# Kernel tuning notes

Measured on AMD Instinct MI355X. Metric: run time of the kernel, lower is better.

Reference implementation:

```python
import jax, jax.numpy as jnp
import numpy as np

N = 12  # mmse_block_size
REAL_SIZE = N * (N + 1) // 2  # 78: diag + strict lower
IMAG_SIZE = N * (N - 1) // 2  # 66: strict lower only
ROWS, COLS = jnp.tril_indices(N)        # row-major (i, j<=i) matches torch loop order
ROWS_S, COLS_S = jnp.tril_indices(N, -1)  # strict lower, row-major, matches imag loop
DIAG_MASK = jnp.eye(N, dtype=bool)


def _mlp(x, W1, b1, W2, b2, W3, b3):
    h = jax.nn.relu(x @ W1 + b1)
    h = jax.nn.relu(h @ W2 + b2)
    return h @ W3 + b3


def _cholesky_outer(flat):
    # flat: [B, REAL_SIZE + IMAG_SIZE] -> [B, N, N] complex, L @ L^H
    B = flat.shape[0]
    L_real = jnp.zeros((B, N, N), flat.dtype).at[:, ROWS, COLS].set(flat[:, :REAL_SIZE])
    L_real = jnp.where(DIAG_MASK, jax.nn.softplus(L_real), L_real)
    L_imag = jnp.zeros((B, N, N), flat.dtype).at[:, ROWS_S, COLS_S].set(
        flat[:, REAL_SIZE:REAL_SIZE + IMAG_SIZE])
    L = L_real + 1j * L_imag
    return jnp.einsum('bij,bkj->bik', L, jnp.conj(L))


def setup_inputs() -> dict:
    key = jax.random.key(0)
    ks = jax.random.split(key, 13)
    L, H, OUT = 4096, 64, REAL_SIZE + IMAG_SIZE
    sc = lambda k, shp, fan: (jax.random.normal(k, shp, jnp.float32) / np.sqrt(fan))
    return {
        'channel_stats': jax.random.normal(ks[0], (8192, L), jnp.float32),
        'WC1': sc(ks[1], (L, H), L), 'bC1': jnp.zeros((H,), jnp.float32),
        'WC2': sc(ks[2], (H, H), H), 'bC2': jnp.zeros((H,), jnp.float32),
        'WC3': sc(ks[3], (H, OUT), H), 'bC3': jnp.zeros((OUT,), jnp.float32),
        'WR1': sc(ks[4], (L, H), L), 'bR1': jnp.zeros((H,), jnp.float32),
        'WR2': sc(ks[5], (H, H), H), 'bR2': jnp.zeros((H,), jnp.float32),
        'WR3': sc(ks[6], (H, OUT), H), 'bR3': jnp.zeros((OUT,), jnp.float32),
    }


def reference(channel_stats, WC1, bC1, WC2, bC2, WC3, bC3,
              WR1, bR1, WR2, bR2, WR3, bR3):
    C_flat = _mlp(channel_stats, WC1, bC1, WC2, bC2, WC3, bC3)
    R_flat = _mlp(channel_stats, WR1, bR1, WR2, bR2, WR3, bR3)
    C = _cholesky_outer(C_flat)
    R = _cholesky_outer(R_flat)
    return C, R
```

## Files before the change

### kernel.cpp

```cpp
#include <hip/hip_runtime.h>
#include <stdint.h>

#define M_ROWS 8192
#define K_DIM  4096
#define OUTD   144
#define PLANE  1179648
#define NT2    8

typedef __attribute__((ext_vector_type(4))) float  float4v;
typedef __attribute__((ext_vector_type(8))) short  short8v;

static __device__ __forceinline__ unsigned short f2bf(float f) {
    unsigned int u = __builtin_bit_cast(unsigned int, f);
    u += 0x7FFFu + ((u >> 16) & 1u);
    return (unsigned short)(u >> 16);
}

__global__ __launch_bounds__(256) void wt_kernel(
    const float* __restrict__ WC1, const float* __restrict__ WR1,
    unsigned short* __restrict__ Wt) {
    __shared__ float tile[64][65];
    const float* src = (blockIdx.y == 0) ? WC1 : WR1;
    const int k0 = blockIdx.x * 64;
    const int t = threadIdx.x;
    const int j = t & 63, qq = t >> 6;
#pragma unroll
    for (int p = 0; p < 16; ++p) {
        int i = p * 4 + qq;
        tile[i][j] = src[(size_t)(k0 + i) * 64 + j];
    }
    __syncthreads();
    const int tt  = blockIdx.x >> 1;
    const int ksb = (blockIdx.x & 1) * 2;
#pragma unroll
    for (int p = 0; p < 16; ++p) {
        int c = p * 256 + t;
        int e = c & 7, m = (c >> 3) & 15, q = (c >> 7) & 3;
        int ks_l = (c >> 9) & 1, w_l = (c >> 10) & 3;
        int kp = ks_l * 32 + q * 8 + e;
        int np = w_l * 16 + m;
        int wg = blockIdx.y * 4 + w_l;
        size_t dst = ((size_t)(wg * 32 + tt) * 4 + (ksb + ks_l)) * 512
                   + q * 128 + m * 8 + e;
        Wt[dst] = f2bf(tile[kp][np]);
    }
}


#define ISSUE_B(TB_, B0_, B1_, B2_, B3_)                         \
    do { const unsigned short* bp_ = bpw + (size_t)(TB_) * 2048; \
         B0_ = *(const short8v*)(bp_ + 0 * 512);                 \
         B1_ = *(const short8v*)(bp_ + 1 * 512);                 \
         B2_ = *(const short8v*)(bp_ + 2 * 512);                 \
         B3_ = *(const short8v*)(bp_ + 3 * 512); } while (0)

#define ISSUE_A(T_, XA_, XB_, XC_, XD_)                          \
    do { const float* ap_ = xpw + (size_t)(T_) * 512;            \
         XA_ = *(const float4*)(ap_);                            \
         XB_ = *(const float4*)(ap_ + 4);                        \
         XC_ = *(const float4*)(ap_ + 256);                      \
         XD_ = *(const float4*)(ap_ + 260); } while (0)

#define STORE_A(BUF_, XA_, XB_, XC_, XD_)                              \
    do { short8v s1_, s2_;                                             \
         s1_[0] = (short)f2bf((XA_).x); s1_[1] = (short)f2bf((XA_).y); \
         s1_[2] = (short)f2bf((XA_).z); s1_[3] = (short)f2bf((XA_).w); \
         s1_[4] = (short)f2bf((XB_).x); s1_[5] = (short)f2bf((XB_).y); \
         s1_[6] = (short)f2bf((XB_).z); s1_[7] = (short)f2bf((XB_).w); \
         s2_[0] = (short)f2bf((XC_).x); s2_[1] = (short)f2bf((XC_).y); \
         s2_[2] = (short)f2bf((XC_).z); s2_[3] = (short)f2bf((XC_).w); \
         s2_[4] = (short)f2bf((XD_).x); s2_[5] = (short)f2bf((XD_).y); \
         s2_[6] = (short)f2bf((XD_).z); s2_[7] = (short)f2bf((XD_).w); \
         *(short8v*)(Asm_ + (BUF_) * 8192 + (w * 64 + lane) * 8) = s1_; \
         *(short8v*)(Asm_ + (BUF_) * 8192 + 4096 + (w * 64 + lane) * 8) = s2_; } while (0)

#define MFR(BUF_, SUB_, B0_, B1_, B2_, B3_)                                    \
    do { const unsigned short* ab_ = Asm_ + (BUF_) * 8192 + (SUB_) * 2048 + lane * 8; \
         short8v a0_ = *(const short8v*)(ab_ + 0 * 512);                       \
         short8v a1_ = *(const short8v*)(ab_ + 1 * 512);                       \
         short8v a2_ = *(const short8v*)(ab_ + 2 * 512);                       \
         short8v a3_ = *(const short8v*)(ab_ + 3 * 512);                       \
         acc = __builtin_amdgcn_mfma_f32_16x16x32_bf16(a0_, B0_, acc, 0, 0, 0);\
         acc = __builtin_amdgcn_mfma_f32_16x16x32_bf16(a1_, B1_, acc, 0, 0, 0);\
         acc = __builtin_amdgcn_mfma_f32_16x16x32_bf16(a2_, B2_, acc, 0, 0, 0);\
         acc = __builtin_amdgcn_mfma_f32_16x16x32_bf16(a3_, B3_, acc, 0, 0, 0);\
    } while (0)

__global__ __launch_bounds__(512, 8) void gemm1_kernel(
    const float* __restrict__ X, const unsigned short* __restrict__ Wt,
    const float* __restrict__ bC1, const float* __restrict__ bR1,
    unsigned int* __restrict__ O32) {
    __shared__ __align__(16) unsigned short Asm_[2 * 8192];

    const int tid  = threadIdx.x;
    const int lane = tid & 63;
    const int w    = tid >> 6;
    const int r0   = blockIdx.x * 16;
    const int m    = lane & 15, q = lane >> 4;

    float4v acc = {0.f, 0.f, 0.f, 0.f};

    const unsigned short* bpw = Wt + (size_t)w * 32 * 2048 + lane * 8;
    const float* xpw = X + (size_t)(r0 + m) * K_DIM + w * 32 + q * 8;

    short8v b00, b01, b02, b03, b10, b11, b12, b13;
    short8v b20, b21, b22, b23, b30, b31, b32, b33;
    float4 xa0, xa1, xa2, xa3;

    ISSUE_A(0, xa0, xa1, xa2, xa3);

#pragma unroll 1
    for (int t = 0; t < NT2; ++t) {
        const int buf = t & 1;
        STORE_A(buf, xa0, xa1, xa2, xa3);
        if (t + 1 < NT2) ISSUE_A(t + 1, xa0, xa1, xa2, xa3);
        asm volatile("s_waitcnt lgkmcnt(0)" ::: "memory");
        __builtin_amdgcn_s_barrier();
        __builtin_amdgcn_sched_barrier(0);
        ISSUE_B(t * 4 + 0, b00, b01, b02, b03);
        ISSUE_B(t * 4 + 1, b10, b11, b12, b13);
        ISSUE_B(t * 4 + 2, b20, b21, b22, b23);
        ISSUE_B(t * 4 + 3, b30, b31, b32, b33);
        MFR(buf, 0, b00, b01, b02, b03);
        MFR(buf, 1, b10, b11, b12, b13);
        MFR(buf, 2, b20, b21, b22, b23);
        MFR(buf, 3, b30, b31, b32, b33);
    }

    {
        const int c = w * 16 + m;
        const float bv = (c < 64) ? bC1[c] : bR1[c - 64];
#pragma unroll
        for (int i = 0; i < 4; ++i) {
            int r = r0 + q * 4 + i;
            float v = acc[i] + bv; v = v > 0.f ? v : 0.f;
            O32[(size_t)PLANE + (size_t)144 * r + c] =
                __builtin_bit_cast(unsigned int, v);
        }
    }
}

__global__ __launch_bounds__(512, 6) void tail_kernel(
    const float* __restrict__ WC2, const float* __restrict__ bC2,
    const float* __restrict__ WR2, const float* __restrict__ bR2,
    const float* __restrict__ WC3, const float* __restrict__ bC3,
    const float* __restrict__ WR3, const float* __restrict__ bR3,
    unsigned int* __restrict__ O32) {
    __shared__ __align__(16) char smem[41216];
    float* hs  = (float*)smem;
    float* W2s = hs + 16 * 132;
    float* fl  = W2s;

    const int tid = threadIdx.x;
    const int r0  = blockIdx.x * 16;

    {
        int row = tid >> 5, qd = tid & 31;
        const float* h1p =
            (const float*)(O32 + (size_t)PLANE + (size_t)144 * (r0 + row));
        *(float4*)&hs[row * 132 + qd * 4] = *(const float4*)(h1p + qd * 4);
    }
#pragma unroll
    for (int p = 0; p < 4; ++p) {
        int fi = p * 512 + tid;
        int k = fi >> 5, c4 = fi & 31;
        int c = c4 * 4;
        const float* wsrc = (c < 64) ? (WC2 + (size_t)k * 64 + c)
                                     : (WR2 + (size_t)k * 64 + (c - 64));
        *(float4*)&W2s[k * 128 + c] = *(const float4*)wsrc;
    }
    __syncthreads();

    const int rg = tid >> 5;
    const int cg = tid & 31;
    const int koff2 = (cg < 16) ? 0 : 64;
    float acc2[4];
    {
        int c = cg * 4;
        const float* bsrc = (c < 64) ? (bC2 + c) : (bR2 + (c - 64));
#pragma unroll
        for (int j = 0; j < 4; ++j) acc2[j] = bsrc[j];
    }
    for (int k = 0; k < 64; ++k) {
        float4 wv = *(const float4*)&W2s[k * 128 + cg * 4];
        float a = hs[rg * 132 + koff2 + k];
        acc2[0] += a * wv.x; acc2[1] += a * wv.y;
        acc2[2] += a * wv.z; acc2[3] += a * wv.w;
    }
    float4 h2v;
    h2v.x = acc2[0] > 0.f ? acc2[0] : 0.f;
    h2v.y = acc2[1] > 0.f ? acc2[1] : 0.f;
    h2v.z = acc2[2] > 0.f ? acc2[2] : 0.f;
    h2v.w = acc2[3] > 0.f ? acc2[3] : 0.f;
    __syncthreads();
    *(float4*)&hs[rg * 132 + cg * 4] = h2v;
    __syncthreads();

#pragma unroll 1
    for (int pass = 0; pass < 3; ++pass) {
        int c = pass * 128 + cg * 4;
        if (c < 288) {
            const int brn = (c >= 144);
            const int cl = c - (brn ? 144 : 0);
            const float* W3 = brn ? WR3 : WC3;
            const float* b3 = brn ? bR3 : bC3;
            const int ko = brn ? 64 : 0;
            float a3[4];
#pragma unroll
            for (int j = 0; j < 4; ++j) a3[j] = b3[cl + j];
            for (int k = 0; k < 64; ++k) {
                float4 wv = *(const float4*)(W3 + (size_t)k * OUTD + cl);
                float a = hs[rg * 132 + ko + k];
                a3[0] += a * wv.x; a3[1] += a * wv.y;
                a3[2] += a * wv.z; a3[3] += a * wv.w;
            }
            float4 v; v.x = a3[0]; v.y = a3[1]; v.z = a3[2]; v.w = a3[3];
            *(float4*)&fl[rg * 288 + c] = v;
        }
    }
    __syncthreads();

    if (tid < 384) {
        int r = tid / 24, rem = tid % 24;
        int brn = rem / 12, ii = rem % 12;
        float* f = &fl[r * 288 + brn * 144];
        int d = ii * (ii + 1) / 2 + ii;
        float xv = f[d];
        f[d] = (xv > 20.f) ? xv : log1pf(expf(xv));
    }
    __syncthreads();

    for (int task = tid; task < 16 * 2 * 78; task += 512) {
        int r = task / 156, rem = task % 156;
        int brn = rem / 78, p = rem % 78;
        int i = 0;
        while (p >= (i + 1) * (i + 2) / 2) ++i;
        int j = p - i * (i + 1) / 2;
        const float* f = &fl[r * 288 + brn * 144];
        const float* g = f + 78;
        const int ti = i * (i + 1) / 2, tj = j * (j + 1) / 2;
        const int si = i * (i - 1) / 2, sj = j * (j - 1) / 2;
        float re = 0.f, im = 0.f;
        for (int k = 0; k <= j; ++k) {
            float ar_ = f[ti + k];
            float ai  = (k == i) ? 0.f : g[si + k];
            float br_ = f[tj + k];
            float bi  = (k == j) ? 0.f : g[sj + k];
            re += ar_ * br_ + ai * bi;
            im += ai * br_ - ar_ * bi;
        }
        unsigned int reb = (unsigned int)f2bf(re);
        unsigned int imb = (unsigned int)f2bf(im);
        unsigned int imn = (unsigned int)f2bf(-im);
        size_t base = brn ? (size_t)PLANE : 0;
        size_t q1 = (size_t)(r0 + r) * 144 + (size_t)(i * 12 + j);
        O32[base + q1] = imb | (reb << 16);
        if (i != j) {
            size_t q2 = (size_t)(r0 + r) * 144 + (size_t)(j * 12 + i);
            O32[base + q2] = imn | (reb << 16);
        }
    }
}

extern "C" void kernel_launch(void* const* d_in, const int* in_sizes, int n_in,
                              void* d_out, int out_size, void* d_ws, size_t ws_size,
                              hipStream_t stream) {
    const float* X   = (const float*)d_in[0];
    const float* WC1 = (const float*)d_in[1];
    const float* bC1 = (const float*)d_in[2];
    const float* WC2 = (const float*)d_in[3];
    const float* bC2 = (const float*)d_in[4];
    const float* WC3 = (const float*)d_in[5];
    const float* bC3 = (const float*)d_in[6];
    const float* WR1 = (const float*)d_in[7];
    const float* bR1 = (const float*)d_in[8];
    const float* WR2 = (const float*)d_in[9];
    const float* bR2 = (const float*)d_in[10];
    const float* WR3 = (const float*)d_in[11];
    const float* bR3 = (const float*)d_in[12];

    unsigned short* Wt  = (unsigned short*)d_ws;
    unsigned int*   O32 = (unsigned int*)d_out;

    wt_kernel<<<dim3(64, 2), 256, 0, stream>>>(WC1, WR1, Wt);
    gemm1_kernel<<<M_ROWS / 16, 512, 0, stream>>>(X, Wt, bC1, bR1, O32);
    tail_kernel<<<M_ROWS / 16, 512, 0, stream>>>(
        WC2, bC2, WR2, bR2, WC3, bC3, WR3, bR3, O32);
}
```

Measured before the change: 272.6 us.

## Retile first GEMM to 128-row tiles with split-K partials reduced in tail

The first-layer GEMM now gives each block a 128-row by 512-K chunk instead of 16 rows over the full K. Each weight fragment is reused across eight row sub-tiles, which cuts repeated B-matrix global loads. A split-K over eight chunks keeps the grid at 512 blocks. Partial sums go to a workspace buffer and the tail kernel adds them, then applies bias and ReLU. The cost is extra global traffic for the partials (8×8192×128 floats written and read) and fewer waves per SIMD, since launch bounds drop from 8 to 4.

```diff
diff --git a/kernel.cpp b/kernel.cpp
--- a/kernel.cpp
+++ b/kernel.cpp
@@ -5,7 +5,8 @@
 #define K_DIM  4096
 #define OUTD   144
 #define PLANE  1179648
-#define NT2    8
+#define KCH    8
+#define NSTEP  8
 
 typedef __attribute__((ext_vector_type(4))) float  float4v;
 typedef __attribute__((ext_vector_type(8))) short  short8v;
@@ -47,100 +48,105 @@
 }
 
 
-#define ISSUE_B(TB_, B0_, B1_, B2_, B3_)                         \
-    do { const unsigned short* bp_ = bpw + (size_t)(TB_) * 2048; \
-         B0_ = *(const short8v*)(bp_ + 0 * 512);                 \
-         B1_ = *(const short8v*)(bp_ + 1 * 512);                 \
-         B2_ = *(const short8v*)(bp_ + 2 * 512);                 \
-         B3_ = *(const short8v*)(bp_ + 3 * 512); } while (0)
-
-#define ISSUE_A(T_, XA_, XB_, XC_, XD_)                          \
-    do { const float* ap_ = xpw + (size_t)(T_) * 512;            \
-         XA_ = *(const float4*)(ap_);                            \
-         XB_ = *(const float4*)(ap_ + 4);                        \
-         XC_ = *(const float4*)(ap_ + 256);                      \
-         XD_ = *(const float4*)(ap_ + 260); } while (0)
-
-#define STORE_A(BUF_, XA_, XB_, XC_, XD_)                              \
+#define ISSUE_AX(S_, X0_, X1_, X2_, X3_)                       \
+    do { const float* ap_ = xpw + (S_) * 64;                   \
+         X0_ = *(const float4*)(ap_);                          \
+         X1_ = *(const float4*)(ap_ + 4);                      \
+         X2_ = *(const float4*)(ap_ + 32);                     \
+         X3_ = *(const float4*)(ap_ + 36); } while (0)
+
+#define STORE_AX(BUF_, X0_, X1_, X2_, X3_)                             \
     do { short8v s1_, s2_;                                             \
-         s1_[0] = (short)f2bf((XA_).x); s1_[1] = (short)f2bf((XA_).y); \
-         s1_[2] = (short)f2bf((XA_).z); s1_[3] = (short)f2bf((XA_).w); \
-         s1_[4] = (short)f2bf((XB_).x); s1_[5] = (short)f2bf((XB_).y); \
-         s1_[6] = (short)f2bf((XB_).z); s1_[7] = (short)f2bf((XB_).w); \
-         s2_[0] = (short)f2bf((XC_).x); s2_[1] = (short)f2bf((XC_).y); \
-         s2_[2] = (short)f2bf((XC_).z); s2_[3] = (short)f2bf((XC_).w); \
-         s2_[4] = (short)f2bf((XD_).x); s2_[5] = (short)f2bf((XD_).y); \
-         s2_[6] = (short)f2bf((XD_).z); s2_[7] = (short)f2bf((XD_).w); \
-         *(short8v*)(Asm_ + (BUF_) * 8192 + (w * 64 + lane) * 8) = s1_; \
-         *(short8v*)(Asm_ + (BUF_) * 8192 + 4096 + (w * 64 + lane) * 8) = s2_; } while (0)
-
-#define MFR(BUF_, SUB_, B0_, B1_, B2_, B3_)                                    \
-    do { const unsigned short* ab_ = Asm_ + (BUF_) * 8192 + (SUB_) * 2048 + lane * 8; \
-         short8v a0_ = *(const short8v*)(ab_ + 0 * 512);                       \
-         short8v a1_ = *(const short8v*)(ab_ + 1 * 512);                       \
-         short8v a2_ = *(const short8v*)(ab_ + 2 * 512);                       \
-         short8v a3_ = *(const short8v*)(ab_ + 3 * 512);                       \
-         acc = __builtin_amdgcn_mfma_f32_16x16x32_bf16(a0_, B0_, acc, 0, 0, 0);\
-         acc = __builtin_amdgcn_mfma_f32_16x16x32_bf16(a1_, B1_, acc, 0, 0, 0);\
-         acc = __builtin_amdgcn_mfma_f32_16x16x32_bf16(a2_, B2_, acc, 0, 0, 0);\
-         acc = __builtin_amdgcn_mfma_f32_16x16x32_bf16(a3_, B3_, acc, 0, 0, 0);\
-    } while (0)
-
-__global__ __launch_bounds__(512, 8) void gemm1_kernel(
+         s1_[0] = (short)f2bf((X0_).x); s1_[1] = (short)f2bf((X0_).y); \
+         s1_[2] = (short)f2bf((X0_).z); s1_[3] = (short)f2bf((X0_).w); \
+         s1_[4] = (short)f2bf((X1_).x); s1_[5] = (short)f2bf((X1_).y); \
+         s1_[6] = (short)f2bf((X1_).z); s1_[7] = (short)f2bf((X1_).w); \
+         s2_[0] = (short)f2bf((X2_).x); s2_[1] = (short)f2bf((X2_).y); \
+         s2_[2] = (short)f2bf((X2_).z); s2_[3] = (short)f2bf((X2_).w); \
+         s2_[4] = (short)f2bf((X3_).x); s2_[5] = (short)f2bf((X3_).y); \
+         s2_[6] = (short)f2bf((X3_).z); s2_[7] = (short)f2bf((X3_).w); \
+         *(short8v*)(awp + (BUF_) * 8192) = s1_;                       \
+         *(short8v*)(awp + (BUF_) * 8192 + 512) = s2_; } while (0)
+
+#define ISSUE_B2(S_, B0_, B1_)                                   \
+    do { const unsigned short* bp_ = bpw + (size_t)(2 * (S_)) * 512; \
+         B0_ = *(const short8v*)(bp_);                           \
+         B1_ = *(const short8v*)(bp_ + 512); } while (0)
+
+#define MFR2(BUF_, B0_, B1_)                                                   \
+    do { _Pragma("unroll")                                                     \
+         for (int rb = 0; rb < 8; ++rb) {                                      \
+             const unsigned short* ab_ = Asm_ + (BUF_) * 8192 + rb * 1024 + lane * 8; \
+             short8v a0_ = *(const short8v*)(ab_);                             \
+             short8v a1_ = *(const short8v*)(ab_ + 512);                       \
+             acc[rb] = __builtin_amdgcn_mfma_f32_16x16x32_bf16(a0_, B0_, acc[rb], 0, 0, 0); \
+             acc[rb] = __builtin_amdgcn_mfma_f32_16x16x32_bf16(a1_, B1_, acc[rb], 0, 0, 0); \
+         } } while (0)
+
+__global__ __launch_bounds__(512, 4) void gemm1_kernel(
     const float* __restrict__ X, const unsigned short* __restrict__ Wt,
-    const float* __restrict__ bC1, const float* __restrict__ bR1,
-    unsigned int* __restrict__ O32) {
+    float* __restrict__ PART) {
     __shared__ __align__(16) unsigned short Asm_[2 * 8192];
 
     const int tid  = threadIdx.x;
     const int lane = tid & 63;
     const int w    = tid >> 6;
-    const int r0   = blockIdx.x * 16;
     const int m    = lane & 15, q = lane >> 4;
-
-    float4v acc = {0.f, 0.f, 0.f, 0.f};
-
-    const unsigned short* bpw = Wt + (size_t)w * 32 * 2048 + lane * 8;
-    const float* xpw = X + (size_t)(r0 + m) * K_DIM + w * 32 + q * 8;
-
-    short8v b00, b01, b02, b03, b10, b11, b12, b13;
-    short8v b20, b21, b22, b23, b30, b31, b32, b33;
+    const int mt   = blockIdx.x & 63;
+    const int kc   = blockIdx.x >> 6;
+    const int r0   = mt * 128;
+
+    const int srow = tid & 127, sq8 = tid >> 7;
+    const float* xpw = X + (size_t)(r0 + srow) * K_DIM + kc * 512 + sq8 * 8;
+    unsigned short* awp = Asm_ + (srow >> 4) * 1024 + (16 * sq8 + (srow & 15)) * 8;
+
+    const unsigned short* bpw = Wt + (size_t)(w * 128 + kc * 16) * 512 + lane * 8;
+
+    float4v acc[8];
+#pragma unroll
+    for (int rb = 0; rb < 8; ++rb) acc[rb] = (float4v){0.f, 0.f, 0.f, 0.f};
+
     float4 xa0, xa1, xa2, xa3;
-
-    ISSUE_A(0, xa0, xa1, xa2, xa3);
+    short8v bA0, bA1, bB0, bB1;
+
+    ISSUE_AX(0, xa0, xa1, xa2, xa3);
+    ISSUE_B2(0, bA0, bA1);
 
 #pragma unroll 1
-    for (int t = 0; t < NT2; ++t) {
-        const int buf = t & 1;
-        STORE_A(buf, xa0, xa1, xa2, xa3);
-        if (t + 1 < NT2) ISSUE_A(t + 1, xa0, xa1, xa2, xa3);
+    for (int sp = 0; sp < NSTEP / 2; ++sp) {
+        const int s = sp * 2;
+        STORE_AX(0, xa0, xa1, xa2, xa3);
+        ISSUE_AX(s + 1, xa0, xa1, xa2, xa3);
         asm volatile("s_waitcnt lgkmcnt(0)" ::: "memory");
         __builtin_amdgcn_s_barrier();
         __builtin_amdgcn_sched_barrier(0);
-        ISSUE_B(t * 4 + 0, b00, b01, b02, b03);
-        ISSUE_B(t * 4 + 1, b10, b11, b12, b13);
-        ISSUE_B(t * 4 + 2, b20, b21, b22, b23);
-        ISSUE_B(t * 4 + 3, b30, b31, b32, b33);
-        MFR(buf, 0, b00, b01, b02, b03);
-        MFR(buf, 1, b10, b11, b12, b13);
-        MFR(buf, 2, b20, b21, b22, b23);
-        MFR(buf, 3, b30, b31, b32, b33);
+        ISSUE_B2(s + 1, bB0, bB1);
+        MFR2(0, bA0, bA1);
+        STORE_AX(1, xa0, xa1, xa2, xa3);
+        if (s + 2 < NSTEP) ISSUE_AX(s + 2, xa0, xa1, xa2, xa3);
+        asm volatile("s_waitcnt lgkmcnt(0)" ::: "memory");
+        __builtin_amdgcn_s_barrier();
+        __builtin_amdgcn_sched_barrier(0);
+        if (s + 2 < NSTEP) ISSUE_B2(s + 2, bA0, bA1);
+        MFR2(1, bB0, bB1);
     }
 
     {
-        const int c = w * 16 + m;
-        const float bv = (c < 64) ? bC1[c] : bR1[c - 64];
-#pragma unroll
-        for (int i = 0; i < 4; ++i) {
-            int r = r0 + q * 4 + i;
-            float v = acc[i] + bv; v = v > 0.f ? v : 0.f;
-            O32[(size_t)PLANE + (size_t)144 * r + c] =
-                __builtin_bit_cast(unsigned int, v);
-        }
+        float* Pf = PART + (size_t)kc * (M_ROWS * 128);
+        const int col = w * 16 + m;
+#pragma unroll
+        for (int rb = 0; rb < 8; ++rb)
+#pragma unroll
+            for (int i = 0; i < 4; ++i) {
+                int grow = r0 + rb * 16 + q * 4 + i;
+                Pf[(size_t)grow * 128 + col] = acc[rb][i];
+            }
     }
 }
 
 __global__ __launch_bounds__(512, 6) void tail_kernel(
+    const float* __restrict__ PART,
+    const float* __restrict__ bC1, const float* __restrict__ bR1,
     const float* __restrict__ WC2, const float* __restrict__ bC2,
     const float* __restrict__ WR2, const float* __restrict__ bR2,
     const float* __restrict__ WC3, const float* __restrict__ bC3,
@@ -155,10 +161,20 @@
     const int r0  = blockIdx.x * 16;
 
     {
-        int row = tid >> 5, qd = tid & 31;
-        const float* h1p =
-            (const float*)(O32 + (size_t)PLANE + (size_t)144 * (r0 + row));
-        *(float4*)&hs[row * 132 + qd * 4] = *(const float4*)(h1p + qd * 4);
+        int r = tid >> 5, c4 = tid & 31;
+        const float* p0 = PART + (size_t)(r0 + r) * 128 + c4 * 4;
+        float4 s = *(const float4*)(p0);
+#pragma unroll
+        for (int kc = 1; kc < KCH; ++kc) {
+            float4 v = *(const float4*)(p0 + (size_t)kc * (M_ROWS * 128));
+            s.x += v.x; s.y += v.y; s.z += v.z; s.w += v.w;
+        }
+        int c = c4 * 4;
+        const float* bsrc = (c < 64) ? (bC1 + c) : (bR1 + (c - 64));
+        s.x += bsrc[0]; s.y += bsrc[1]; s.z += bsrc[2]; s.w += bsrc[3];
+        s.x = s.x > 0.f ? s.x : 0.f;  s.y = s.y > 0.f ? s.y : 0.f;
+        s.z = s.z > 0.f ? s.z : 0.f;  s.w = s.w > 0.f ? s.w : 0.f;
+        *(float4*)&hs[r * 132 + c] = s;
     }
 #pragma unroll
     for (int p = 0; p < 4; ++p) {
@@ -280,10 +296,11 @@
     const float* bR3 = (const float*)d_in[12];
 
     unsigned short* Wt  = (unsigned short*)d_ws;
-    unsigned int*   O32 = (unsigned int*)d_out;
+    float* PART = (float*)((char*)d_ws + (2u << 20));
+    unsigned int* O32 = (unsigned int*)d_out;
 
     wt_kernel<<<dim3(64, 2), 256, 0, stream>>>(WC1, WR1, Wt);
-    gemm1_kernel<<<M_ROWS / 16, 512, 0, stream>>>(X, Wt, bC1, bR1, O32);
+    gemm1_kernel<<<64 * KCH, 512, 0, stream>>>(X, Wt, PART);
     tail_kernel<<<M_ROWS / 16, 512, 0, stream>>>(
-        WC2, bC2, WR2, bR2, WC3, bC3, WR3, bR3, O32);
-}
+        PART, bC1, bR1, WC2, bC2, WR2, bR2, WC3, bC3, WR3, bR3, O32);
+}
```

Result: no change. 273.1 us (+0.2%).
